# Optimization experiments

Hardware: AMD Instinct MI355X
Metric: run time of the kernel (lower is better)

Reference implementation:

```python
import jax, jax.numpy as jnp
import numpy as np

K, D = 512, 2048
B, T = 32, 512

def setup_inputs() -> dict:
    key = jax.random.key(0)
    k1, k2, k3, k4 = jax.random.split(key, 4)
    z_e_x = jax.random.normal(k1, (B, D, T), dtype=jnp.float32)
    # embedding.weight.data.uniform_(-1/K, 1/K)
    codebook = jax.random.uniform(k2, (K, D), dtype=jnp.float32, minval=-1.0 / K, maxval=1.0 / K)
    # Conv1d(2048, 1, 1): weight (1, 2048, 1) -> stored as (D,), bias (1,)
    bound = 1.0 / np.sqrt(D)
    conv_w = jax.random.uniform(k3, (D,), dtype=jnp.float32, minval=-bound, maxval=bound)
    conv_b = jax.random.uniform(k4, (1,), dtype=jnp.float32, minval=-bound, maxval=bound)
    return {"z_e_x": z_e_x, "codebook": codebook, "conv_w": conv_w, "conv_b": conv_b}

def _vq_indices(flat, codebook):
    # flat: (N, D), codebook: (K, D); squared L2 distances via expansion
    dists = (
        jnp.sum(flat * flat, axis=1, keepdims=True)
        - 2.0 * flat @ codebook.T
        + jnp.sum(codebook * codebook, axis=1)[None, :]
    )  # (N, K)
    return jnp.argmin(dists, axis=1)  # (N,)

def _conv1x1(x, conv_w, conv_b):
    # Conv1d(D, 1, kernel=1) on (B, D, T) -> (B, 1, T)
    return jnp.einsum('bdt,d->bt', x, conv_w)[:, None, :] + conv_b[None, :, None]

def reference(z_e_x, codebook, conv_w, conv_b):
    # Faithful to VQEmbedding.straight_through (superset of forward's vq)
    z = jnp.transpose(z_e_x, (0, 2, 1))            # (B, T, D)
    flat = z.reshape(-1, D)                         # (N, D)
    indices = _vq_indices(flat, codebook)           # (N,) == forward()'s latents (flattened)
    quant = codebook[indices].reshape(z.shape)      # (B, T, D)
    # vq_st: straight-through estimator (codebook detached, grad copies to z_e_x)
    z_q_ = z + jax.lax.stop_gradient(quant - z)
    z_q_x = jnp.transpose(z_q_, (0, 2, 1))          # (B, D, T)
    z_q_x_onehot = _conv1x1(z_q_x, conv_w, conv_b)  # (B, 1, T)
    # index_select on non-detached embedding weight -> grads flow to codebook here
    z_q_x_bar = jnp.transpose(quant, (0, 2, 1))     # (B, D, T)
    z_q_x_bar_onehot = _conv1x1(z_q_x_bar, conv_w, conv_b)
    return (z_q_x, z_q_x_onehot, z_q_x_bar, z_q_x_bar_onehot)
```

## Files before the change

kernel.cpp:

```cpp
#include <hip/hip_runtime.h>
#include <cstdint>

#define Dd 2048
#define Tt 512
#define Bb 32
#define Kc 512
#define Nn 16384

typedef _Float16 half8 __attribute__((ext_vector_type(8)));
typedef float f32x4 __attribute__((ext_vector_type(4)));

__device__ __forceinline__ float sqf(float v) { return v * v; }

__device__ __forceinline__ unsigned int fenc(float f) {
  unsigned int u = __float_as_uint(f);
  return (u & 0x80000000u) ? ~u : (u | 0x80000000u);
}

__device__ __forceinline__ unsigned long long ullmin(unsigned long long a,
                                                     unsigned long long b) {
  return b < a ? b : a;
}


__global__ __launch_bounds__(256) void k_splitz(const float* __restrict__ z,
                                                _Float16* __restrict__ zh,
                                                _Float16* __restrict__ zl,
                                                float* __restrict__ Bc) {
  __shared__ float sbuf[64 * 130];
  __shared__ float Ps[4 * 64];
  const int tid = threadIdx.x;
  const int t0  = blockIdx.x * 64;
  const int b   = blockIdx.y;
  const int cg  = blockIdx.z;
  const int tt  = tid & 63;
  const int w   = tid >> 6;

  for (int ci = 0; ci < 4; ++ci) {
    const int c = cg * 4 + ci;
    const float* zp = z + (size_t)b * Dd * Tt + (size_t)(c * 128) * Tt + t0;
    __syncthreads();
    #pragma unroll
    for (int i = 0; i < 32; ++i) {
      const int d = i * 4 + w;
      sbuf[tt * 130 + d] = zp[(size_t)d * Tt + tt];
    }
    __syncthreads();
    {
      const float* row = &sbuf[tt * 130];
      const int j = 2 * w;
      float r0 = sqf(row[j]);
      float r1 = sqf(row[j + 1]);
      #pragma unroll
      for (int s = 1; s < 16; ++s) {
        r0 += sqf(row[j + 8 * s]);
        r1 += sqf(row[j + 1 + 8 * s]);
      }
      Ps[w * 64 + tt] = r0 + r1;
    }
    {
      const int chunk = tid & 15;
      const int rr    = tid >> 4;
      #pragma unroll
      for (int p = 0; p < 4; ++p) {
        const int t = p * 16 + rr;
        const float* src = &sbuf[t * 130 + chunk * 8];
        __align__(16) _Float16 hbuf[8], lbuf[8];
        #pragma unroll
        for (int jj = 0; jj < 8; ++jj) {
          float v = src[jj];
          _Float16 h = (_Float16)v;
          hbuf[jj] = h;
          lbuf[jj] = (_Float16)((v - (float)h) * 4096.f);
        }
        const size_t off = (size_t)(b * Tt + t0 + t) * Dd + c * 128 + chunk * 8;
        *(float4*)(zh + off) = *(float4*)hbuf;
        *(float4*)(zl + off) = *(float4*)lbuf;
      }
    }
    __syncthreads();
    if (tid < 64) {
      const float B = (Ps[tid] + Ps[64 + tid]) + (Ps[128 + tid] + Ps[192 + tid]);
      Bc[c * Nn + b * Tt + t0 + tid] = B;
    }
  }
}

__global__ __launch_bounds__(256) void k_xcomb(const float* __restrict__ Bc,
                                               float* __restrict__ xnorm) {
  int n = blockIdx.x * 256 + threadIdx.x;
  float bb[16];
  #pragma unroll
  for (int c = 0; c < 16; ++c) bb[c] = Bc[c * Nn + n];
  float d0 = (bb[0] + bb[1]) + (bb[2] + bb[3]);
  float d1 = (bb[4] + bb[5]) + (bb[6] + bb[7]);
  float d2 = (bb[8] + bb[9]) + (bb[10] + bb[11]);
  float d3 = (bb[12] + bb[13]) + (bb[14] + bb[15]);
  xnorm[n] = (d0 + d1) + (d2 + d3);
}

__global__ __launch_bounds__(256) void k_prep2(const float* __restrict__ cb,
                                               const float* __restrict__ w,
                                               float* __restrict__ cnorm,
                                               float* __restrict__ qd,
                                               _Float16* __restrict__ chp,
                                               _Float16* __restrict__ clp) {
  __shared__ float Bs[16 * 16];
  __shared__ float Qs[16 * 16];
  const int tid = threadIdx.x;
  const int kl  = tid >> 4;
  const int blk = tid & 15;
  const int k = blockIdx.x * 16 + kl;
  const float* row = cb + (size_t)k * Dd + blk * 128;
  const float* wp  = w + blk * 128;
  _Float16* ch_o = chp + (size_t)k * Dd + blk * 128;
  _Float16* cl_o = clp + (size_t)k * Dd + blk * 128;
  __align__(16) _Float16 hbuf[8], lbuf[8];
  float r[8];
  float q = 0.f;
  for (int s = 0; s < 16; ++s) {
    #pragma unroll
    for (int j = 0; j < 8; ++j) {
      int p = s * 8 + j;
      float v = row[p];
      float sq = v * v;
      if (s == 0) r[j] = sq; else r[j] += sq;
      q = fmaf(v, wp[p], q);
      _Float16 h = (_Float16)v;
      hbuf[j] = h;
      lbuf[j] = (_Float16)((v - (float)h) * 4096.f);
    }
    *(float4*)(ch_o + s * 8) = *(float4*)hbuf;
    *(float4*)(cl_o + s * 8) = *(float4*)lbuf;
  }
  float B = ((r[0] + r[1]) + (r[2] + r[3])) + ((r[4] + r[5]) + (r[6] + r[7]));
  Bs[kl * 16 + blk] = B;
  Qs[kl * 16 + blk] = q;
  __syncthreads();
  if (blk == 0) {
    const float* bb = &Bs[kl * 16];
    float d0 = (bb[0] + bb[1]) + (bb[2] + bb[3]);
    float d1 = (bb[4] + bb[5]) + (bb[6] + bb[7]);
    float d2 = (bb[8] + bb[9]) + (bb[10] + bb[11]);
    float d3 = (bb[12] + bb[13]) + (bb[14] + bb[15]);
    cnorm[k] = (d0 + d1) + (d2 + d3);
    const float* qq = &Qs[kl * 16];
    float s = 0.f;
    #pragma unroll
    for (int i = 0; i < 16; ++i) s += qq[i];
    qd[k] = s;
  }
}

__global__ __launch_bounds__(256) void k_prep_nb(const float* __restrict__ cb,
                                                 const float* __restrict__ w,
                                                 float* __restrict__ cnorm,
                                                 float* __restrict__ qd) {
  __shared__ float Bs[16 * 16];
  __shared__ float Qs[16 * 16];
  const int tid = threadIdx.x;
  const int kl  = tid >> 4;
  const int blk = tid & 15;
  const int k = blockIdx.x * 16 + kl;
  const float* row = cb + (size_t)k * Dd + blk * 128;
  const float* wp  = w + blk * 128;
  float r[8];
  float q = 0.f;
  for (int s = 0; s < 16; ++s) {
    #pragma unroll
    for (int j = 0; j < 8; ++j) {
      int p = s * 8 + j;
      float v = row[p];
      float sq = v * v;
      if (s == 0) r[j] = sq; else r[j] += sq;
      q = fmaf(v, wp[p], q);
    }
  }
  float B = ((r[0] + r[1]) + (r[2] + r[3])) + ((r[4] + r[5]) + (r[6] + r[7]));
  Bs[kl * 16 + blk] = B;
  Qs[kl * 16 + blk] = q;
  __syncthreads();
  if (blk == 0) {
    const float* bb = &Bs[kl * 16];
    float d0 = (bb[0] + bb[1]) + (bb[2] + bb[3]);
    float d1 = (bb[4] + bb[5]) + (bb[6] + bb[7]);
    float d2 = (bb[8] + bb[9]) + (bb[10] + bb[11]);
    float d3 = (bb[12] + bb[13]) + (bb[14] + bb[15]);
    cnorm[k] = (d0 + d1) + (d2 + d3);
    const float* qq = &Qs[kl * 16];
    float s = 0.f;
    #pragma unroll
    for (int i = 0; i < 16; ++i) s += qq[i];
    qd[k] = s;
  }
}

__global__ __launch_bounds__(256, 2) void k_gemm_mfma(
    const _Float16* __restrict__ zh, const _Float16* __restrict__ zl,
    const _Float16* __restrict__ ch, const _Float16* __restrict__ cl,
    const float* __restrict__ xnorm, const float* __restrict__ cnorm,
    unsigned long long* __restrict__ keys) {
  const int n0 = blockIdx.x * 128;
  const int k0 = blockIdx.y * 128;

  __shared__ __align__(16) float lds[4 * 128 * 20];
  float* Ah = lds;
  float* Al = lds + 2560;
  float* Bh = lds + 5120;
  float* Bl = lds + 7680;
  __shared__ unsigned long long keybuf[128][2];

  const int tid  = threadIdx.x;
  const int r    = tid >> 2;
  const int q    = tid & 3;
  const int lane = tid & 63;
  const int wid  = tid >> 6;
  const int wr   = wid >> 1, wc = wid & 1;
  const int lrow = lane & 15, lq = lane >> 4;

  f32x4 acc_h[4][4], acc_x[4][4];
  #pragma unroll
  for (int i = 0; i < 4; ++i)
    #pragma unroll
    for (int j = 0; j < 4; ++j) {
      acc_h[i][j] = (f32x4)0.f;
      acc_x[i][j] = (f32x4)0.f;
    }

  const _Float16* gAh = zh + (size_t)(n0 + r) * Dd + q * 8;
  const _Float16* gAl = zl + (size_t)(n0 + r) * Dd + q * 8;
  const _Float16* gBh = ch + (size_t)(k0 + r) * Dd + q * 8;
  const _Float16* gBl = cl + (size_t)(k0 + r) * Dd + q * 8;
  const size_t rowskip = (size_t)64 * Dd;

  float4 pAh0 = *(const float4*)(gAh);
  float4 pAh1 = *(const float4*)(gAh + rowskip);
  float4 pAl0 = *(const float4*)(gAl);
  float4 pAl1 = *(const float4*)(gAl + rowskip);
  float4 pBh0 = *(const float4*)(gBh);
  float4 pBh1 = *(const float4*)(gBh + rowskip);
  float4 pBl0 = *(const float4*)(gBl);
  float4 pBl1 = *(const float4*)(gBl + rowskip);

  const int wa0 = r * 20 + q * 4;
  const int wa1 = (r + 64) * 20 + q * 4;

  for (int dt = 0; dt < Dd / 32; ++dt) {
    __syncthreads();
    *(float4*)&Ah[wa0] = pAh0;  *(float4*)&Ah[wa1] = pAh1;
    *(float4*)&Al[wa0] = pAl0;  *(float4*)&Al[wa1] = pAl1;
    *(float4*)&Bh[wa0] = pBh0;  *(float4*)&Bh[wa1] = pBh1;
    *(float4*)&Bl[wa0] = pBl0;  *(float4*)&Bl[wa1] = pBl1;
    __syncthreads();
    if (dt + 1 < Dd / 32) {
      const int off = (dt + 1) * 32;
      pAh0 = *(const float4*)(gAh + off);
      pAh1 = *(const float4*)(gAh + rowskip + off);
      pAl0 = *(const float4*)(gAl + off);
      pAl1 = *(const float4*)(gAl + rowskip + off);
      pBh0 = *(const float4*)(gBh + off);
      pBh1 = *(const float4*)(gBh + rowskip + off);
      pBl0 = *(const float4*)(gBl + off);
      pBl1 = *(const float4*)(gBl + rowskip + off);
    }
    half8 ah[4], al[4];
    #pragma unroll
    for (int i = 0; i < 4; ++i) {
      int row = wr * 64 + i * 16 + lrow;
      ah[i] = *(half8*)&Ah[row * 20 + lq * 4];
      al[i] = *(half8*)&Al[row * 20 + lq * 4];
    }
    #pragma unroll
    for (int j = 0; j < 4; ++j) {
      int row = wc * 64 + j * 16 + lrow;
      half8 bh = *(half8*)&Bh[row * 20 + lq * 4];
      half8 bl = *(half8*)&Bl[row * 20 + lq * 4];
      #pragma unroll
      for (int i = 0; i < 4; ++i) {
        acc_h[i][j] = __builtin_amdgcn_mfma_f32_16x16x32_f16(ah[i], bh, acc_h[i][j], 0, 0, 0);
        acc_x[i][j] = __builtin_amdgcn_mfma_f32_16x16x32_f16(ah[i], bl, acc_x[i][j], 0, 0, 0);
        acc_x[i][j] = __builtin_amdgcn_mfma_f32_16x16x32_f16(al[i], bh, acc_x[i][j], 0, 0, 0);
      }
    }
  }

  float cn[4];
  #pragma unroll
  for (int j = 0; j < 4; ++j) cn[j] = cnorm[k0 + wc * 64 + j * 16 + lrow];

  #pragma unroll
  for (int i = 0; i < 4; ++i) {
    #pragma unroll
    for (int reg = 0; reg < 4; ++reg) {
      const int rowl = wr * 64 + i * 16 + lq * 4 + reg;
      const float xn = xnorm[n0 + rowl];
      unsigned long long best = ~0ull;
      #pragma unroll
      for (int j = 0; j < 4; ++j) {
        float dot = acc_h[i][j][reg] + acc_x[i][j][reg] * 0x1p-12f;
        float d = fmaf(-2.f, dot, xn) + cn[j];
        unsigned int code = (unsigned int)(k0 + wc * 64 + j * 16 + lrow);
        unsigned long long key = ((unsigned long long)fenc(d) << 32) | code;
        best = ullmin(best, key);
      }
      #pragma unroll
      for (int m = 1; m < 16; m <<= 1)
        best = ullmin(best, (unsigned long long)__shfl_xor((unsigned long long)best, m, 64));
      if (lrow == 0) keybuf[rowl][wc] = best;
    }
  }
  __syncthreads();
  if (tid < 128) {
    unsigned long long kk = ullmin(keybuf[tid][0], keybuf[tid][1]);
    atomicMin(&keys[n0 + tid], kk);
  }
}

__global__ __launch_bounds__(256) void k_final(const unsigned long long* __restrict__ keys,
                                               const float* __restrict__ qd,
                                               const float* __restrict__ bconv,
                                               int* __restrict__ idxb,
                                               float* __restrict__ out1,
                                               float* __restrict__ out3) {
  int n = blockIdx.x * 256 + threadIdx.x;
  unsigned long long key = keys[n];
  int k = (int)(key & 0xFFFFFFFFull);
  idxb[n] = k;
  float v = qd[k] + bconv[0];
  out1[n] = v;
  out3[n] = v;
}

__global__ __launch_bounds__(256) void k_scatter(const float* __restrict__ cb,
                                                 const int* __restrict__ idxb,
                                                 float* __restrict__ out0,
                                                 float* __restrict__ out2) {
  const int d0 = blockIdx.x * 16;
  const int b  = blockIdx.y;
  __shared__ float cb_s[512 * 17];
  const int tid = threadIdx.x;
  {
    const int kk = tid >> 2;
    const int dq = tid & 3;
    #pragma unroll
    for (int p = 0; p < 8; ++p) {
      int k = p * 64 + kk;
      float4 v = *(const float4*)(cb + (size_t)k * Dd + d0 + dq * 4);
      cb_s[k * 17 + dq * 4 + 0] = v.x;
      cb_s[k * 17 + dq * 4 + 1] = v.y;
      cb_s[k * 17 + dq * 4 + 2] = v.z;
      cb_s[k * 17 + dq * 4 + 3] = v.w;
    }
  }
  const int t4 = (tid & 127) * 4;
  int4 idx4 = *(const int4*)(idxb + b * Tt + t4);
  __syncthreads();
  const int dhalf = tid >> 7;
  #pragma unroll
  for (int p = 0; p < 8; ++p) {
    int dd = p * 2 + dhalf;
    float4 o;
    o.x = cb_s[idx4.x * 17 + dd];
    o.y = cb_s[idx4.y * 17 + dd];
    o.z = cb_s[idx4.z * 17 + dd];
    o.w = cb_s[idx4.w * 17 + dd];
    size_t off = (size_t)b * Dd * Tt + (size_t)(d0 + dd) * Tt + t4;
    *(float4*)(out0 + off) = o;
    *(float4*)(out2 + off) = o;
  }
}


__global__ __launch_bounds__(256) void k_xnorm(const float* __restrict__ z,
                                               float* __restrict__ xnorm) {
  const int t0 = blockIdx.x * 64;
  const int b  = blockIdx.y;
  __shared__ float sbuf[128 * 64];
  __shared__ float Ps[256];
  __shared__ float Bs2[64 * 16];
  const int tid = threadIdx.x;
  const int tt = tid & 63;
  const int j2 = tid >> 6;
  const float* zb = z + (size_t)b * Dd * Tt + t0;
  for (int c = 0; c < 16; ++c) {
    __syncthreads();
    #pragma unroll
    for (int it = 0; it < 32; ++it) {
      int d = j2 + it * 4;
      sbuf[d * 64 + tt] = zb[(size_t)(c * 128 + d) * Tt + tt];
    }
    __syncthreads();
    float r0, r1;
    {
      const int j = 2 * j2;
      r0 = sqf(sbuf[j * 64 + tt]);
      #pragma unroll
      for (int s = 1; s < 16; ++s) r0 += sqf(sbuf[(j + 8 * s) * 64 + tt]);
      r1 = sqf(sbuf[(j + 1) * 64 + tt]);
      #pragma unroll
      for (int s = 1; s < 16; ++s) r1 += sqf(sbuf[(j + 1 + 8 * s) * 64 + tt]);
    }
    Ps[j2 * 64 + tt] = r0 + r1;
    __syncthreads();
    if (tid < 64) {
      float B = (Ps[tid] + Ps[64 + tid]) + (Ps[128 + tid] + Ps[192 + tid]);
      Bs2[tid * 16 + c] = B;
    }
  }
  __syncthreads();
  if (tid < 64) {
    const float* bb = &Bs2[tid * 16];
    float d0 = (bb[0] + bb[1]) + (bb[2] + bb[3]);
    float d1 = (bb[4] + bb[5]) + (bb[6] + bb[7]);
    float d2 = (bb[8] + bb[9]) + (bb[10] + bb[11]);
    float d3 = (bb[12] + bb[13]) + (bb[14] + bb[15]);
    xnorm[b * Tt + t0 + tid] = (d0 + d1) + (d2 + d3);
  }
}

__global__ __launch_bounds__(256, 2) void k_gemm(const float* __restrict__ z,
                                                 const float* __restrict__ cb,
                                                 const float* __restrict__ cnorm,
                                                 const float* __restrict__ xnorm,
                                                 unsigned long long* __restrict__ keys) {
  const int n0 = blockIdx.x * 128;
  const int k0 = blockIdx.y * 128;
  const int b  = n0 >> 9;
  const int t0 = n0 & 511;
  const float* zbase = z + (size_t)b * Dd * Tt + t0;

  __shared__ __align__(16) float As[32 * 132];
  __shared__ __align__(16) float Cs[32 * 132];
  __shared__ float red_v[16 * 128];
  __shared__ int   red_i[16 * 128];

  const int tid = threadIdx.x;
  const int t4a = (tid & 31) * 4;
  const int dla = tid >> 5;
  const int kc  = tid >> 3;
  const int dq  = tid & 7;
  const int r0  = (tid & 15) * 8;
  const int c0  = (tid >> 4) * 8;

  float4 pa[4], pc[4];
  {
    #pragma unroll
    for (int p = 0; p < 4; ++p)
      pa[p] = *(const float4*)(zbase + (size_t)(dla + p * 8) * Tt + t4a);
    const float* cp = cb + (size_t)(k0 + kc) * Dd + dq * 4;
    #pragma unroll
    for (int p = 0; p < 4; ++p)
      pc[p] = *(const float4*)(cp + (size_t)p * 32 * Dd);
  }

  float acc[8][8];
  #pragma unroll
  for (int i = 0; i < 8; ++i)
    #pragma unroll
    for (int j = 0; j < 8; ++j) acc[i][j] = 0.f;

  for (int dt = 0; dt < Dd / 32; ++dt) {
    __syncthreads();
    #pragma unroll
    for (int p = 0; p < 4; ++p)
      *(float4*)&As[(dla + p * 8) * 132 + t4a] = pa[p];
    #pragma unroll
    for (int p = 0; p < 4; ++p) {
      Cs[(dq * 4 + 0) * 132 + kc + p * 32] = pc[p].x;
      Cs[(dq * 4 + 1) * 132 + kc + p * 32] = pc[p].y;
      Cs[(dq * 4 + 2) * 132 + kc + p * 32] = pc[p].z;
      Cs[(dq * 4 + 3) * 132 + kc + p * 32] = pc[p].w;
    }
    __syncthreads();
    if (dt + 1 < Dd / 32) {
      const float* zp = zbase + (size_t)(dt + 1) * 32 * Tt;
      #pragma unroll
      for (int p = 0; p < 4; ++p)
        pa[p] = *(const float4*)(zp + (size_t)(dla + p * 8) * Tt + t4a);
      const float* cp = cb + (size_t)(k0 + kc) * Dd + (dt + 1) * 32 + dq * 4;
      #pragma unroll
      for (int p = 0; p < 4; ++p)
        pc[p] = *(const float4*)(cp + (size_t)p * 32 * Dd);
    }
    #pragma unroll 8
    for (int dl = 0; dl < 32; ++dl) {
      float4 a0 = *(const float4*)&As[dl * 132 + r0];
      float4 a1 = *(const float4*)&As[dl * 132 + r0 + 4];
      float4 b0 = *(const float4*)&Cs[dl * 132 + c0];
      float4 b1 = *(const float4*)&Cs[dl * 132 + c0 + 4];
      float av[8] = {a0.x, a0.y, a0.z, a0.w, a1.x, a1.y, a1.z, a1.w};
      float bv[8] = {b0.x, b0.y, b0.z, b0.w, b1.x, b1.y, b1.z, b1.w};
      #pragma unroll
      for (int i = 0; i < 8; ++i)
        #pragma unroll
        for (int j = 0; j < 8; ++j)
          acc[i][j] = fmaf(av[i], bv[j], acc[i][j]);
    }
  }

  float cn[8];
  #pragma unroll
  for (int j = 0; j < 8; ++j) cn[j] = cnorm[k0 + c0 + j];
  float xnv[8];
  #pragma unroll
  for (int i = 0; i < 8; ++i) xnv[i] = xnorm[n0 + r0 + i];

  const int c16 = tid >> 4;
  #pragma unroll
  for (int i = 0; i < 8; ++i) {
    float bv = fmaf(-2.f, acc[i][0], xnv[i]) + cn[0];
    int bi = 0;
    #pragma unroll
    for (int j = 1; j < 8; ++j) {
      float d = fmaf(-2.f, acc[i][j], xnv[i]) + cn[j];
      if (d < bv) { bv = d; bi = j; }
    }
    red_v[c16 * 128 + r0 + i] = bv;
    red_i[c16 * 128 + r0 + i] = k0 + c0 + bi;
  }
  __syncthreads();
  if (tid < 128) {
    float bv = red_v[tid];
    int bi = red_i[tid];
    #pragma unroll
    for (int j = 1; j < 16; ++j) {
      float v = red_v[j * 128 + tid];
      if (v < bv) { bv = v; bi = red_i[j * 128 + tid]; }
    }
    unsigned long long key = ((unsigned long long)fenc(bv) << 32) | (unsigned int)bi;
    atomicMin(&keys[n0 + tid], key);
  }
}


extern "C" void kernel_launch(void* const* d_in, const int* in_sizes, int n_in,
                              void* d_out, int out_size, void* d_ws, size_t ws_size,
                              hipStream_t stream) {
  const float* z  = (const float*)d_in[0];
  const float* cb = (const float*)d_in[1];
  const float* w  = (const float*)d_in[2];
  const float* bc = (const float*)d_in[3];

  float* out0 = (float*)d_out;
  float* out1 = out0 + (size_t)Bb * Dd * Tt;
  float* out2 = out1 + (size_t)Bb * Tt;
  float* out3 = out2 + (size_t)Bb * Dd * Tt;

  char* ws = (char*)d_ws;
  unsigned long long* keys = (unsigned long long*)ws;
  float* cnorm = (float*)(ws + 131072);
  float* qd    = (float*)(ws + 133120);
  int*   idxb  = (int*)(ws + 135168);
  float* xnorm = (float*)(ws + 200704);
  float* Bc    = (float*)(ws + 266240);
  _Float16* chp = (_Float16*)(ws + 1314816);
  _Float16* clp = (_Float16*)(ws + 3411968);
  _Float16* zh  = (_Float16*)(ws + 5509120);
  _Float16* zl  = (_Float16*)(ws + 72617984);
  const size_t need = 139726848;

  hipMemsetAsync(keys, 0xFF, (size_t)Nn * 8, stream);

  if (ws_size >= need) {
    k_splitz<<<dim3(Tt / 64, Bb, 4), dim3(256), 0, stream>>>(z, zh, zl, Bc);
    k_prep2<<<dim3(Kc / 16), dim3(256), 0, stream>>>(cb, w, cnorm, qd, chp, clp);
    k_xcomb<<<dim3(Nn / 256), dim3(256), 0, stream>>>(Bc, xnorm);
    k_gemm_mfma<<<dim3(Nn / 128, Kc / 128), dim3(256), 0, stream>>>(
        zh, zl, chp, clp, xnorm, cnorm, keys);
  } else {
    k_xnorm<<<dim3(Tt / 64, Bb), dim3(256), 0, stream>>>(z, xnorm);
    k_prep_nb<<<dim3(Kc / 16), dim3(256), 0, stream>>>(cb, w, cnorm, qd);
    k_gemm<<<dim3(Nn / 128, Kc / 128), dim3(256), 0, stream>>>(z, cb, cnorm, xnorm, keys);
  }
  k_final<<<dim3(Nn / 256), dim3(256), 0, stream>>>(keys, qd, bc, idxb, out1, out3);
  k_scatter<<<dim3(Dd / 16, Bb), dim3(256), 0, stream>>>(cb, idxb, out0, out2);
}
```

Measured before the change: 547.5 us.

## Use direct global-to-LDS loads in GEMM and fuse xnorm/final into neighbors

The GEMM tile loads now go straight from global memory into LDS with global_load_lds, replacing the register-staged prefetch. The LDS layout becomes unpadded, 32 halves per row, and launch bounds are raised to 3 blocks per CU. The xnorm combine kernel is folded into the GEMM prologue, and the final index/conv kernel is folded into the scatter kernel, which removes two launches and their global round-trips. The cost is that the register prefetch overlap is lost, so loads are now exposed between barriers. The unpadded LDS rows may also cause bank conflicts, and raising the occupancy target could cause register spills.

Measured after the change: 600.2 us. +9.6%, slower.

```diff
diff --git a/kernel.cpp b/kernel.cpp
--- a/kernel.cpp
+++ b/kernel.cpp
@@ -20,6 +20,12 @@
 __device__ __forceinline__ unsigned long long ullmin(unsigned long long a,
                                                      unsigned long long b) {
   return b < a ? b : a;
+}
+
+__device__ __forceinline__ void gload_lds16(const _Float16* g, _Float16* l) {
+  __builtin_amdgcn_global_load_lds(
+      (const __attribute__((address_space(1))) void*)g,
+      (__attribute__((address_space(3))) void*)l, 16, 0, 0);
 }
 
 
@@ -86,19 +92,6 @@
   }
 }
 
-__global__ __launch_bounds__(256) void k_xcomb(const float* __restrict__ Bc,
-                                               float* __restrict__ xnorm) {
-  int n = blockIdx.x * 256 + threadIdx.x;
-  float bb[16];
-  #pragma unroll
-  for (int c = 0; c < 16; ++c) bb[c] = Bc[c * Nn + n];
-  float d0 = (bb[0] + bb[1]) + (bb[2] + bb[3]);
-  float d1 = (bb[4] + bb[5]) + (bb[6] + bb[7]);
-  float d2 = (bb[8] + bb[9]) + (bb[10] + bb[11]);
-  float d3 = (bb[12] + bb[13]) + (bb[14] + bb[15]);
-  xnorm[n] = (d0 + d1) + (d2 + d3);
-}
-
 __global__ __launch_bounds__(256) void k_prep2(const float* __restrict__ cb,
                                                const float* __restrict__ w,
                                                float* __restrict__ cnorm,
@@ -195,24 +188,32 @@
   }
 }
 
-__global__ __launch_bounds__(256, 2) void k_gemm_mfma(
+__global__ __launch_bounds__(256, 3) void k_gemm_mfma(
     const _Float16* __restrict__ zh, const _Float16* __restrict__ zl,
     const _Float16* __restrict__ ch, const _Float16* __restrict__ cl,
-    const float* __restrict__ xnorm, const float* __restrict__ cnorm,
+    const float* __restrict__ Bc, const float* __restrict__ cnorm,
     unsigned long long* __restrict__ keys) {
   const int n0 = blockIdx.x * 128;
   const int k0 = blockIdx.y * 128;
 
-  __shared__ __align__(16) float lds[4 * 128 * 20];
-  float* Ah = lds;
-  float* Al = lds + 2560;
-  float* Bh = lds + 5120;
-  float* Bl = lds + 7680;
+  __shared__ __align__(16) _Float16 smem[4 * 128 * 32];
   __shared__ unsigned long long keybuf[128][2];
-
-  const int tid  = threadIdx.x;
-  const int r    = tid >> 2;
-  const int q    = tid & 3;
+  __shared__ float xn_s[128];
+
+  const int tid = threadIdx.x;
+
+  if (tid < 128) {
+    const int n = n0 + tid;
+    float bb[16];
+    #pragma unroll
+    for (int c = 0; c < 16; ++c) bb[c] = Bc[c * Nn + n];
+    float d0 = (bb[0] + bb[1]) + (bb[2] + bb[3]);
+    float d1 = (bb[4] + bb[5]) + (bb[6] + bb[7]);
+    float d2 = (bb[8] + bb[9]) + (bb[10] + bb[11]);
+    float d3 = (bb[12] + bb[13]) + (bb[14] + bb[15]);
+    xn_s[tid] = (d0 + d1) + (d2 + d3);
+  }
+
   const int lane = tid & 63;
   const int wid  = tid >> 6;
   const int wr   = wid >> 1, wc = wid & 1;
@@ -227,54 +228,45 @@
       acc_x[i][j] = (f32x4)0.f;
     }
 
-  const _Float16* gAh = zh + (size_t)(n0 + r) * Dd + q * 8;
-  const _Float16* gAl = zl + (size_t)(n0 + r) * Dd + q * 8;
-  const _Float16* gBh = ch + (size_t)(k0 + r) * Dd + q * 8;
-  const _Float16* gBl = cl + (size_t)(k0 + r) * Dd + q * 8;
-  const size_t rowskip = (size_t)64 * Dd;
-
-  float4 pAh0 = *(const float4*)(gAh);
-  float4 pAh1 = *(const float4*)(gAh + rowskip);
-  float4 pAl0 = *(const float4*)(gAl);
-  float4 pAl1 = *(const float4*)(gAl + rowskip);
-  float4 pBh0 = *(const float4*)(gBh);
-  float4 pBh1 = *(const float4*)(gBh + rowskip);
-  float4 pBl0 = *(const float4*)(gBl);
-  float4 pBl1 = *(const float4*)(gBl + rowskip);
-
-  const int wa0 = r * 20 + q * 4;
-  const int wa1 = (r + 64) * 20 + q * 4;
+  const int srow = tid >> 2;
+  const int scol = (tid & 3) * 8;
+  const _Float16* gsrc0 = zh + (size_t)(n0 + srow) * Dd + scol;
+  const _Float16* gsrc1 = zl + (size_t)(n0 + srow) * Dd + scol;
+  const _Float16* gsrc2 = ch + (size_t)(k0 + srow) * Dd + scol;
+  const _Float16* gsrc3 = cl + (size_t)(k0 + srow) * Dd + scol;
+  _Float16* ldst = smem + tid * 8;
+
+  const _Float16* Ah = smem;
+  const _Float16* Al = smem + 4096;
+  const _Float16* Bh = smem + 8192;
+  const _Float16* Bl = smem + 12288;
+  const size_t half_skip = (size_t)64 * Dd;
 
   for (int dt = 0; dt < Dd / 32; ++dt) {
-    __syncthreads();
-    *(float4*)&Ah[wa0] = pAh0;  *(float4*)&Ah[wa1] = pAh1;
-    *(float4*)&Al[wa0] = pAl0;  *(float4*)&Al[wa1] = pAl1;
-    *(float4*)&Bh[wa0] = pBh0;  *(float4*)&Bh[wa1] = pBh1;
-    *(float4*)&Bl[wa0] = pBl0;  *(float4*)&Bl[wa1] = pBl1;
-    __syncthreads();
-    if (dt + 1 < Dd / 32) {
-      const int off = (dt + 1) * 32;
-      pAh0 = *(const float4*)(gAh + off);
-      pAh1 = *(const float4*)(gAh + rowskip + off);
-      pAl0 = *(const float4*)(gAl + off);
-      pAl1 = *(const float4*)(gAl + rowskip + off);
-      pBh0 = *(const float4*)(gBh + off);
-      pBh1 = *(const float4*)(gBh + rowskip + off);
-      pBl0 = *(const float4*)(gBl + off);
-      pBl1 = *(const float4*)(gBl + rowskip + off);
-    }
+    const int doff = dt * 32;
+    __syncthreads();
+    gload_lds16(gsrc0 + doff,             ldst);
+    gload_lds16(gsrc0 + half_skip + doff, ldst + 2048);
+    gload_lds16(gsrc1 + doff,             ldst + 4096);
+    gload_lds16(gsrc1 + half_skip + doff, ldst + 6144);
+    gload_lds16(gsrc2 + doff,             ldst + 8192);
+    gload_lds16(gsrc2 + half_skip + doff, ldst + 10240);
+    gload_lds16(gsrc3 + doff,             ldst + 12288);
+    gload_lds16(gsrc3 + half_skip + doff, ldst + 14336);
+    __syncthreads();
+
     half8 ah[4], al[4];
     #pragma unroll
     for (int i = 0; i < 4; ++i) {
       int row = wr * 64 + i * 16 + lrow;
-      ah[i] = *(half8*)&Ah[row * 20 + lq * 4];
-      al[i] = *(half8*)&Al[row * 20 + lq * 4];
+      ah[i] = *(const half8*)&Ah[row * 32 + lq * 8];
+      al[i] = *(const half8*)&Al[row * 32 + lq * 8];
     }
     #pragma unroll
     for (int j = 0; j < 4; ++j) {
       int row = wc * 64 + j * 16 + lrow;
-      half8 bh = *(half8*)&Bh[row * 20 + lq * 4];
-      half8 bl = *(half8*)&Bl[row * 20 + lq * 4];
+      half8 bh = *(const half8*)&Bh[row * 32 + lq * 8];
+      half8 bl = *(const half8*)&Bl[row * 32 + lq * 8];
       #pragma unroll
       for (int i = 0; i < 4; ++i) {
         acc_h[i][j] = __builtin_amdgcn_mfma_f32_16x16x32_f16(ah[i], bh, acc_h[i][j], 0, 0, 0);
@@ -293,7 +285,7 @@
     #pragma unroll
     for (int reg = 0; reg < 4; ++reg) {
       const int rowl = wr * 64 + i * 16 + lq * 4 + reg;
-      const float xn = xnorm[n0 + rowl];
+      const float xn = xn_s[rowl];
       unsigned long long best = ~0ull;
       #pragma unroll
       for (int j = 0; j < 4; ++j) {
@@ -316,25 +308,14 @@
   }
 }
 
-__global__ __launch_bounds__(256) void k_final(const unsigned long long* __restrict__ keys,
-                                               const float* __restrict__ qd,
-                                               const float* __restrict__ bconv,
-                                               int* __restrict__ idxb,
-                                               float* __restrict__ out1,
-                                               float* __restrict__ out3) {
-  int n = blockIdx.x * 256 + threadIdx.x;
-  unsigned long long key = keys[n];
-  int k = (int)(key & 0xFFFFFFFFull);
-  idxb[n] = k;
-  float v = qd[k] + bconv[0];
-  out1[n] = v;
-  out3[n] = v;
-}
-
 __global__ __launch_bounds__(256) void k_scatter(const float* __restrict__ cb,
-                                                 const int* __restrict__ idxb,
+                                                 const unsigned long long* __restrict__ keys,
+                                                 const float* __restrict__ qd,
+                                                 const float* __restrict__ bconv,
                                                  float* __restrict__ out0,
-                                                 float* __restrict__ out2) {
+                                                 float* __restrict__ out1,
+                                                 float* __restrict__ out2,
+                                                 float* __restrict__ out3) {
   const int d0 = blockIdx.x * 16;
   const int b  = blockIdx.y;
   __shared__ float cb_s[512 * 17];
@@ -353,7 +334,22 @@
     }
   }
   const int t4 = (tid & 127) * 4;
-  int4 idx4 = *(const int4*)(idxb + b * Tt + t4);
+  const unsigned long long* kp = keys + b * Tt + t4;
+  int4 idx4;
+  idx4.x = (int)(kp[0] & 0xFFFFFFFFull);
+  idx4.y = (int)(kp[1] & 0xFFFFFFFFull);
+  idx4.z = (int)(kp[2] & 0xFFFFFFFFull);
+  idx4.w = (int)(kp[3] & 0xFFFFFFFFull);
+  if (blockIdx.x == 0 && tid < 128) {
+    const float bc0 = bconv[0];
+    float4 o1;
+    o1.x = qd[idx4.x] + bc0;
+    o1.y = qd[idx4.y] + bc0;
+    o1.z = qd[idx4.z] + bc0;
+    o1.w = qd[idx4.w] + bc0;
+    *(float4*)(out1 + b * Tt + t4) = o1;
+    *(float4*)(out3 + b * Tt + t4) = o1;
+  }
   __syncthreads();
   const int dhalf = tid >> 7;
   #pragma unroll
@@ -550,7 +546,6 @@
   unsigned long long* keys = (unsigned long long*)ws;
   float* cnorm = (float*)(ws + 131072);
   float* qd    = (float*)(ws + 133120);
-  int*   idxb  = (int*)(ws + 135168);
   float* xnorm = (float*)(ws + 200704);
   float* Bc    = (float*)(ws + 266240);
   _Float16* chp = (_Float16*)(ws + 1314816);
@@ -564,14 +559,13 @@
   if (ws_size >= need) {
     k_splitz<<<dim3(Tt / 64, Bb, 4), dim3(256), 0, stream>>>(z, zh, zl, Bc);
     k_prep2<<<dim3(Kc / 16), dim3(256), 0, stream>>>(cb, w, cnorm, qd, chp, clp);
-    k_xcomb<<<dim3(Nn / 256), dim3(256), 0, stream>>>(Bc, xnorm);
     k_gemm_mfma<<<dim3(Nn / 128, Kc / 128), dim3(256), 0, stream>>>(
-        zh, zl, chp, clp, xnorm, cnorm, keys);
+        zh, zl, chp, clp, Bc, cnorm, keys);
   } else {
     k_xnorm<<<dim3(Tt / 64, Bb), dim3(256), 0, stream>>>(z, xnorm);
     k_prep_nb<<<dim3(Kc / 16), dim3(256), 0, stream>>>(cb, w, cnorm, qd);
     k_gemm<<<dim3(Nn / 128, Kc / 128), dim3(256), 0, stream>>>(z, cb, cnorm, xnorm, keys);
   }
-  k_final<<<dim3(Nn / 256), dim3(256), 0, stream>>>(keys, qd, bc, idxb, out1, out3);
-  k_scatter<<<dim3(Dd / 16, Bb), dim3(256), 0, stream>>>(cb, idxb, out0, out2);
-}
+  k_scatter<<<dim3(Dd / 16, Bb), dim3(256), 0, stream>>>(cb, keys, qd, bc,
+                                                         out0, out1, out2, out3);
+}
```
